# Kernel tuning notes

Measured on AMD Instinct MI355X. Metric: run time of the kernel, lower is better.

The kernel has to match this reference:

```python
import jax, jax.numpy as jnp
import numpy as np

B, T, C, H = 4, 2048, 1024, 16
HS = C // H  # head_size = 64


def setup_inputs() -> dict:
    key = jax.random.key(0)
    ks = jax.random.split(key, 6)
    s = C ** -0.5  # Linear default init scale (approx, kaiming-uniform-ish)
    x = jax.random.normal(ks[0], (B, T, C), dtype=jnp.float32)
    Wq = jax.random.normal(ks[1], (H, C, HS), dtype=jnp.float32) * s
    Wk = jax.random.normal(ks[2], (H, C, HS), dtype=jnp.float32) * s
    Wv = jax.random.normal(ks[3], (H, C, HS), dtype=jnp.float32) * s
    Wproj = jax.random.normal(ks[4], (C, C), dtype=jnp.float32) * s
    bproj = jax.random.normal(ks[5], (C,), dtype=jnp.float32) * s
    return {"x": x, "Wq": Wq, "Wk": Wk, "Wv": Wv, "Wproj": Wproj, "bproj": bproj}


def reference(x, Wq, Wk, Wv, Wproj, bproj):
    # Batched multi-head attention equivalent to looping over per-head modules.
    # q,k,v: (B, H, T, HS)
    q = jnp.einsum('btc,hcd->bhtd', x, Wq)
    k = jnp.einsum('btc,hcd->bhtd', x, Wk)
    v = jnp.einsum('btc,hcd->bhtd', x, Wv)
    scale = HS ** -0.5
    scores = jnp.einsum('bhqd,bhkd->bhqk', q, k) * scale  # (B,H,T,T)
    causal = jnp.tril(jnp.ones((T, T), dtype=bool))
    scores = jnp.where(causal, scores, -jnp.inf)
    wei = jax.nn.softmax(scores, axis=-1)
    out_heads = jnp.einsum('bhqk,bhkd->bhqd', wei, v)  # (B,H,T,HS)
    # concat heads along last dim -> (B,T,H*HS) = (B,T,C)
    combo = out_heads.transpose(0, 2, 1, 3).reshape(B, T, C)
    out = jnp.einsum('btc,cd->btd', combo, Wproj.T.T @ jnp.eye(C, dtype=combo.dtype)) if False else combo @ Wproj.T + bproj
    # dropout p=0.0 (eval) -> identity
    return out
```

## Files before the change

kernel.cpp:

```cpp
#include <hip/hip_runtime.h>
#include <stdint.h>

#define B_  4
#define T_  2048
#define C_  1024
#define H_  16
#define HS_ 64
#define M_  (B_*T_)
#define K_  C_

typedef unsigned short u16;
typedef float v4f __attribute__((ext_vector_type(4)));
typedef short v8s __attribute__((ext_vector_type(8)));
typedef u16   v4u __attribute__((ext_vector_type(4)));
typedef unsigned int u32;
typedef u32 v2u32 __attribute__((ext_vector_type(2)));

__device__ __forceinline__ u16 f2bf(float f){
  unsigned u = __float_as_uint(f);
  u += 0x7fffu + ((u >> 16) & 1u);
  return (u16)(u >> 16);
}

__device__ __forceinline__ u32 cvt_pk_bf16(float a, float b){
  u32 r;
  asm("v_cvt_pk_bf16_f32 %0, %1, %2" : "=v"(r) : "v"(a), "v"(b));
  return r;
}

__device__ __forceinline__ void async16(const void* g, void* l){
  __builtin_amdgcn_global_load_lds(
      (const __attribute__((address_space(1))) unsigned int*)g,
      (__attribute__((address_space(3))) unsigned int*)l,
      16, 0, 0);
}

__global__ void conv_f32_bf16(const float* __restrict__ src, u16* __restrict__ dst){
  int i = (blockIdx.x * 256 + threadIdx.x) * 4;
  v4f v = *(const v4f*)(src + i);
  v4u o;
  #pragma unroll
  for (int j = 0; j < 4; j++) o[j] = f2bf(v[j]);
  *(v4u*)(dst + i) = o;
}

__global__ void transpose_w(const float* __restrict__ Wq, const float* __restrict__ Wk,
                            const float* __restrict__ Wv, u16* __restrict__ wallT){
  int idx = blockIdx.x * 256 + threadIdx.x;
  int n = idx >> 10, c = idx & 1023;
  int tensor = n >> 10;
  int h = (n >> 6) & 15;
  int d = n & 63;
  const float* W = (tensor == 0) ? Wq : ((tensor == 1) ? Wk : Wv);
  wallT[idx] = f2bf(W[((size_t)(h * C_ + c)) * HS_ + d]);
}

#define QSCALE 0.1803368801111204f

template<int MODE>
__global__ __launch_bounds__(256)
void gemm_bt(const u16* __restrict__ A, const u16* __restrict__ Bt,
             const float* __restrict__ bias,
             u16* __restrict__ o0, u16* __restrict__ o1, u16* __restrict__ o2,
             float* __restrict__ o0f)
{
  __shared__ __align__(16) u16 sA[2][128 * 32];
  __shared__ __align__(16) u16 sB[2][128 * 32];
  const int tid  = threadIdx.x;
  const int lane = tid & 63;
  const int wave = tid >> 6;
  const int l15  = lane & 15, quad = lane >> 4;
  const int wm   = wave >> 1, wn = wave & 1;
  const int m0   = blockIdx.y * 128;
  const int n0   = blockIdx.x * 128;

  v4f acc[4][4] = {};

  const int s0 = tid, s1 = tid + 256;
  const int ar0 = ((s0 >> 6) << 4) + (s0 & 15);
  const int ac0 = ((s0 >> 4) & 3) << 4;
  const int ar1 = ((s1 >> 6) << 4) + (s1 & 15);
  const int ac1 = ((s1 >> 4) & 3) << 4;

  const char* Ab = (const char*)A;
  const char* Bb = (const char*)Bt;

  async16(Ab + ((size_t)(m0 + ar0) * K_) * 2 + ac0, (char*)sA[0] + s0 * 16);
  async16(Ab + ((size_t)(m0 + ar1) * K_) * 2 + ac1, (char*)sA[0] + s1 * 16);
  async16(Bb + ((size_t)(n0 + ar0) * K_) * 2 + ac0, (char*)sB[0] + s0 * 16);
  async16(Bb + ((size_t)(n0 + ar1) * K_) * 2 + ac1, (char*)sB[0] + s1 * 16);
  __syncthreads();

  int cur = 0;
  for (int kk = 0; kk < K_; kk += 32){
    const int nxt = cur ^ 1;
    if (kk + 32 < K_){
      const int k2b = (kk + 32) * 2;
      async16(Ab + ((size_t)(m0 + ar0) * K_) * 2 + k2b + ac0, (char*)sA[nxt] + s0 * 16);
      async16(Ab + ((size_t)(m0 + ar1) * K_) * 2 + k2b + ac1, (char*)sA[nxt] + s1 * 16);
      async16(Bb + ((size_t)(n0 + ar0) * K_) * 2 + k2b + ac0, (char*)sB[nxt] + s0 * 16);
      async16(Bb + ((size_t)(n0 + ar1) * K_) * 2 + k2b + ac1, (char*)sB[nxt] + s1 * 16);
    }

    v8s af[4], bfr[4];
    const u16* pa = sA[cur] + (size_t)(wm * 4) * 512 + lane * 8;
    const u16* pb = sB[cur] + (size_t)(wn * 4) * 512 + lane * 8;
    #pragma unroll
    for (int mi = 0; mi < 4; mi++) af[mi]  = *(const v8s*)(pa + mi * 512);
    #pragma unroll
    for (int ni = 0; ni < 4; ni++) bfr[ni] = *(const v8s*)(pb + ni * 512);

    #pragma unroll
    for (int mi = 0; mi < 4; mi++)
      #pragma unroll
      for (int ni = 0; ni < 4; ni++)
        acc[mi][ni] = __builtin_amdgcn_mfma_f32_16x16x32_bf16(af[mi], bfr[ni], acc[mi][ni], 0, 0, 0);

    __syncthreads();
    cur = nxt;
  }

  if constexpr (MODE == 0){
    #pragma unroll
    for (int ni = 0; ni < 4; ni++){
      const int ng = n0 + wn * 64 + ni * 16 + l15;
      const int tensor = ng >> 10;
      const int hh = (ng >> 6) & 15;
      const int d  = ng & 63;
      #pragma unroll
      for (int mi = 0; mi < 4; mi++){
        const int mbase = m0 + wm * 64 + mi * 16 + quad * 4;
        const int bb = mbase >> 11;
        const int tt = mbase & 2047;
        if (tensor == 2){
          v4u pk;
          #pragma unroll
          for (int r = 0; r < 4; r++) pk[r] = f2bf(acc[mi][ni][r]);
          *(v4u*)(o2 + ((size_t)((bb * H_ + hh) * HS_ + d)) * T_ + tt) = pk;
        } else if (tensor == 0){
          #pragma unroll
          for (int r = 0; r < 4; r++)
            o0[((size_t)((bb * H_ + hh)) * T_ + tt + r) * HS_ + d] = f2bf(acc[mi][ni][r] * QSCALE);
        } else {
          #pragma unroll
          for (int r = 0; r < 4; r++)
            o1[((size_t)((bb * H_ + hh)) * T_ + tt + r) * HS_ + d] = f2bf(acc[mi][ni][r]);
        }
      }
    }
  } else {
    #pragma unroll
    for (int ni = 0; ni < 4; ni++){
      const int ng = n0 + wn * 64 + ni * 16 + l15;
      const float bv = bias[ng];
      #pragma unroll
      for (int mi = 0; mi < 4; mi++){
        const int mbase = m0 + wm * 64 + mi * 16 + quad * 4;
        #pragma unroll
        for (int r = 0; r < 4; r++)
          o0f[(size_t)(mbase + r) * C_ + ng] = acc[mi][ni][r] + bv;
      }
    }
  }
}

__global__ __launch_bounds__(512, 4)
void attn(const u16* __restrict__ Q, const u16* __restrict__ Kb_, const u16* __restrict__ Vt,
          u16* __restrict__ O)
{
  __shared__ __align__(16) u16 sK[64 * 64];
  __shared__ __align__(16) u16 sV[64 * 64];
  __shared__ __align__(16) u16 Plds[8][16][88];
  const int tid  = threadIdx.x;
  const int lane = tid & 63;
  const int wave = tid >> 6;
  const int l15  = lane & 15, quad = lane >> 4;
  const int pp   = blockIdx.y & 7;
  const int bh   = blockIdx.x * 8 + (blockIdx.y >> 3);

  const u16* Qb = Q   + (size_t)bh * T_ * HS_;
  const u16* Kb = Kb_ + (size_t)bh * T_ * HS_;
  const u16* Vb = Vt  + (size_t)bh * HS_ * T_;
  const int b = bh >> 4, h = bh & 15;

  const int g  = tid;
  const int tg = g >> 3;
  const int sw = ((g & 7) ^ (tg & 7)) << 4;
  const char* Kby = (const char*)Kb;
  const char* Vby = (const char*)Vb;
  const int koff = tg * 128 + sw;
  const int voff = tg * (T_ * 2) + sw;
  char* sKp = (char*)sK + g * 16;
  char* sVp = (char*)sV + g * 16;

  const int fsw0 = (quad ^ (l15 & 7)) * 8;
  const int fsw1 = ((quad + 4) ^ (l15 & 7)) * 8;

  #pragma unroll 1
  for (int ph = 0; ph < 2; ph++){
    const int qt = ph ? (15 - pp) : pp;
    const int q0 = qt * 128 + wave * 16;

    const v8s qf0 = *(const v8s*)(Qb + (size_t)(q0 + l15) * HS_ + quad * 8);
    const v8s qf1 = *(const v8s*)(Qb + (size_t)(q0 + l15) * HS_ + 32 + quad * 8);

    v4f Oa[4] = {};
    float lsum = 0.f;

    const int ktmax = 2 * qt + 1;
    for (int kt = 0; kt <= ktmax; kt++){
      const int k0 = kt * 64;
      async16(Kby + (size_t)k0 * 128 + koff, sKp);
      async16(Vby + (size_t)k0 * 2   + voff, sVp);
      __syncthreads();

      if (k0 <= q0 + 15){
        v4f sacc[4] = {};
        __builtin_amdgcn_s_setprio(1);
        #pragma unroll
        for (int nt = 0; nt < 4; nt++){
          const u16* kr = sK + (nt * 16 + l15) * 64;
          v8s kf0 = *(const v8s*)(kr + fsw0);
          v8s kf1 = *(const v8s*)(kr + fsw1);
          sacc[nt] = __builtin_amdgcn_mfma_f32_16x16x32_bf16(kf0, qf0, sacc[nt], 0, 0, 0);
          sacc[nt] = __builtin_amdgcn_mfma_f32_16x16x32_bf16(kf1, qf1, sacc[nt], 0, 0, 0);
        }
        __builtin_amdgcn_s_setprio(0);
        const bool diag = (k0 + 63 > q0);
        const int qrow_rel = (q0 - k0) + l15;

        #pragma unroll
        for (int nt = 0; nt < 4; nt++){
          float p0 = exp2f(sacc[nt][0]);
          float p1 = exp2f(sacc[nt][1]);
          float p2 = exp2f(sacc[nt][2]);
          float p3 = exp2f(sacc[nt][3]);
          if (diag){
            const int kbase = nt * 16 + quad * 4;
            if (kbase + 0 > qrow_rel) p0 = 0.f;
            if (kbase + 1 > qrow_rel) p1 = 0.f;
            if (kbase + 2 > qrow_rel) p2 = 0.f;
            if (kbase + 3 > qrow_rel) p3 = 0.f;
          }
          lsum += (p0 + p1) + (p2 + p3);
          v2u32 w;
          w[0] = cvt_pk_bf16(p0, p1);
          w[1] = cvt_pk_bf16(p2, p3);
          *(v2u32*)&Plds[wave][l15][nt * 16 + quad * 4] = w;
        }

        asm volatile("" ::: "memory");
        const v8s pf0 = *(const v8s*)&Plds[wave][l15][quad * 8];
        const v8s pf1 = *(const v8s*)&Plds[wave][l15][32 + quad * 8];
        __builtin_amdgcn_s_setprio(1);
        #pragma unroll
        for (int nt = 0; nt < 4; nt++){
          const u16* vr = sV + (nt * 16 + l15) * 64;
          v8s vf0 = *(const v8s*)(vr + fsw0);
          v8s vf1 = *(const v8s*)(vr + fsw1);
          Oa[nt] = __builtin_amdgcn_mfma_f32_16x16x32_bf16(pf0, vf0, Oa[nt], 0, 0, 0);
          Oa[nt] = __builtin_amdgcn_mfma_f32_16x16x32_bf16(pf1, vf1, Oa[nt], 0, 0, 0);
        }
        __builtin_amdgcn_s_setprio(0);
      }
      __syncthreads();
    }

    float rs = lsum;
    rs += __shfl_xor(rs, 16);
    rs += __shfl_xor(rs, 32);
    #pragma unroll
    for (int reg = 0; reg < 4; reg++){
      const float rsq = __shfl(rs, quad * 4 + reg);
      const float inv = (rsq > 0.f) ? (1.f / rsq) : 0.f;
      const int t = q0 + quad * 4 + reg;
      #pragma unroll
      for (int nt = 0; nt < 4; nt++)
        O[((size_t)(b * T_ + t)) * C_ + h * HS_ + nt * 16 + l15] = f2bf(Oa[nt][reg] * inv);
    }
  }
}

extern "C" void kernel_launch(void* const* d_in, const int* in_sizes, int n_in,
                              void* d_out, int out_size, void* d_ws, size_t ws_size,
                              hipStream_t stream)
{
  const float* x     = (const float*)d_in[0];
  const float* Wq    = (const float*)d_in[1];
  const float* Wk    = (const float*)d_in[2];
  const float* Wv    = (const float*)d_in[3];
  const float* Wproj = (const float*)d_in[4];
  const float* bproj = (const float*)d_in[5];
  float* out = (float*)d_out;

  u16* xhat   = (u16*)d_ws;
  u16* att    = xhat;
  u16* q_ws   = xhat  + (size_t)M_ * C_;
  u16* k_ws   = q_ws  + (size_t)M_ * C_;
  u16* vt_ws  = k_ws  + (size_t)M_ * C_;
  u16* wallT  = vt_ws + (size_t)M_ * C_;
  u16* wprojT = wallT + (size_t)3 * C_ * K_;

  conv_f32_bf16<<<dim3((M_ * C_) / 1024), dim3(256), 0, stream>>>(x, xhat);
  transpose_w<<<dim3((3 * C_ * K_) / 256), dim3(256), 0, stream>>>(Wq, Wk, Wv, wallT);
  conv_f32_bf16<<<dim3((C_ * C_) / 1024), dim3(256), 0, stream>>>(Wproj, wprojT);
  gemm_bt<0><<<dim3(24, 64), dim3(256), 0, stream>>>(xhat, wallT, nullptr,
                                                     q_ws, k_ws, vt_ws, nullptr);
  attn<<<dim3(8, 64), dim3(512), 0, stream>>>(q_ws, k_ws, vt_ws, att);
  gemm_bt<1><<<dim3(8, 64), dim3(256), 0, stream>>>(att, wprojT, bproj,
                                                    nullptr, nullptr, nullptr, out);
}
```

Baseline: 308.3 us.

## Store GEMM operands in pre-blocked 16x8 tile layout for contiguous async loads

Changes the bf16 conversion of x and Wproj, the QKV weight transpose, and the attention output write so that operands are stored in a blocked layout: groups of 16 rows by 8 k-elements are contiguous. The GEMM's async global-to-LDS loads then read contiguous 16-byte chunks with a simple per-k-step offset, where before each load was strided by a full row. The aim is better memory coalescing and simpler address arithmetic in the GEMMs. In exchange, the attention output stores and the weight transpose now write scattered 2-byte elements, which may reduce write efficiency there.

```diff
diff --git a/kernel.cpp b/kernel.cpp
--- a/kernel.cpp
+++ b/kernel.cpp
@@ -35,13 +35,18 @@
       16, 0, 0);
 }
 
-__global__ void conv_f32_bf16(const float* __restrict__ src, u16* __restrict__ dst){
-  int i = (blockIdx.x * 256 + threadIdx.x) * 4;
-  v4f v = *(const v4f*)(src + i);
-  v4u o;
-  #pragma unroll
-  for (int j = 0; j < 4; j++) o[j] = f2bf(v[j]);
-  *(v4u*)(dst + i) = o;
+
+__global__ void conv_blocked(const float* __restrict__ src, u16* __restrict__ dst){
+  int gid = blockIdx.x * 256 + threadIdx.x;
+  int r  = gid >> 7;
+  int kg = gid & 127;
+  const float* s = src + ((size_t)r << 10) + (kg << 3);
+  v4f a = *(const v4f*)s;
+  v4f b = *(const v4f*)(s + 4);
+  union { v8s v; u16 e[8]; } o;
+  o.e[0]=f2bf(a[0]); o.e[1]=f2bf(a[1]); o.e[2]=f2bf(a[2]); o.e[3]=f2bf(a[3]);
+  o.e[4]=f2bf(b[0]); o.e[5]=f2bf(b[1]); o.e[6]=f2bf(b[2]); o.e[7]=f2bf(b[3]);
+  *(v8s*)(dst + (((size_t)(r >> 4) * 128 + kg) * 128 + ((r & 15) << 3))) = o.v;
 }
 
 __global__ void transpose_w(const float* __restrict__ Wq, const float* __restrict__ Wk,
@@ -52,7 +57,8 @@
   int h = (n >> 6) & 15;
   int d = n & 63;
   const float* W = (tensor == 0) ? Wq : ((tensor == 1) ? Wk : Wv);
-  wallT[idx] = f2bf(W[((size_t)(h * C_ + c)) * HS_ + d]);
+  wallT[((size_t)(n >> 4) * 128 + (c >> 3)) * 128 + ((n & 15) << 3) + (c & 7)]
+      = f2bf(W[((size_t)(h * C_ + c)) * HS_ + d]);
 }
 
 #define QSCALE 0.1803368801111204f
@@ -73,33 +79,35 @@
   const int wm   = wave >> 1, wn = wave & 1;
   const int m0   = blockIdx.y * 128;
   const int n0   = blockIdx.x * 128;
+  const int mg0  = blockIdx.y * 8;
+  const int ng0  = blockIdx.x * 8;
 
   v4f acc[4][4] = {};
 
   const int s0 = tid, s1 = tid + 256;
-  const int ar0 = ((s0 >> 6) << 4) + (s0 & 15);
-  const int ac0 = ((s0 >> 4) & 3) << 4;
-  const int ar1 = ((s1 >> 6) << 4) + (s1 & 15);
-  const int ac1 = ((s1 >> 4) & 3) << 4;
-
-  const char* Ab = (const char*)A;
-  const char* Bb = (const char*)Bt;
-
-  async16(Ab + ((size_t)(m0 + ar0) * K_) * 2 + ac0, (char*)sA[0] + s0 * 16);
-  async16(Ab + ((size_t)(m0 + ar1) * K_) * 2 + ac1, (char*)sA[0] + s1 * 16);
-  async16(Bb + ((size_t)(n0 + ar0) * K_) * 2 + ac0, (char*)sB[0] + s0 * 16);
-  async16(Bb + ((size_t)(n0 + ar1) * K_) * 2 + ac1, (char*)sB[0] + s1 * 16);
+  const int t0 = s0 >> 6, r0 = s0 & 15, g0 = (s0 >> 4) & 3;
+  const int t1 = s1 >> 6, r1 = s1 & 15, g1 = (s1 >> 4) & 3;
+
+  const char* aS0 = (const char*)A  + ((size_t)(mg0 + t0) * 16384 + g0 * 128 + r0 * 8) * 2;
+  const char* aS1 = (const char*)A  + ((size_t)(mg0 + t1) * 16384 + g1 * 128 + r1 * 8) * 2;
+  const char* bS0 = (const char*)Bt + ((size_t)(ng0 + t0) * 16384 + g0 * 128 + r0 * 8) * 2;
+  const char* bS1 = (const char*)Bt + ((size_t)(ng0 + t1) * 16384 + g1 * 128 + r1 * 8) * 2;
+
+  async16(aS0, (char*)sA[0] + s0 * 16);
+  async16(aS1, (char*)sA[0] + s1 * 16);
+  async16(bS0, (char*)sB[0] + s0 * 16);
+  async16(bS1, (char*)sB[0] + s1 * 16);
   __syncthreads();
 
   int cur = 0;
   for (int kk = 0; kk < K_; kk += 32){
     const int nxt = cur ^ 1;
     if (kk + 32 < K_){
-      const int k2b = (kk + 32) * 2;
-      async16(Ab + ((size_t)(m0 + ar0) * K_) * 2 + k2b + ac0, (char*)sA[nxt] + s0 * 16);
-      async16(Ab + ((size_t)(m0 + ar1) * K_) * 2 + k2b + ac1, (char*)sA[nxt] + s1 * 16);
-      async16(Bb + ((size_t)(n0 + ar0) * K_) * 2 + k2b + ac0, (char*)sB[nxt] + s0 * 16);
-      async16(Bb + ((size_t)(n0 + ar1) * K_) * 2 + k2b + ac1, (char*)sB[nxt] + s1 * 16);
+      const size_t off = (size_t)(kk + 32) * 32;
+      async16(aS0 + off, (char*)sA[nxt] + s0 * 16);
+      async16(aS1 + off, (char*)sA[nxt] + s1 * 16);
+      async16(bS0 + off, (char*)sB[nxt] + s0 * 16);
+      async16(bS1 + off, (char*)sB[nxt] + s1 * 16);
     }
 
     v8s af[4], bfr[4];
@@ -269,14 +277,17 @@
     float rs = lsum;
     rs += __shfl_xor(rs, 16);
     rs += __shfl_xor(rs, 32);
+    const int mg = b * 128 + qt * 8 + wave;
     #pragma unroll
     for (int reg = 0; reg < 4; reg++){
       const float rsq = __shfl(rs, quad * 4 + reg);
       const float inv = (rsq > 0.f) ? (1.f / rsq) : 0.f;
-      const int t = q0 + quad * 4 + reg;
+      const int mrow = quad * 4 + reg;
       #pragma unroll
-      for (int nt = 0; nt < 4; nt++)
-        O[((size_t)(b * T_ + t)) * C_ + h * HS_ + nt * 16 + l15] = f2bf(Oa[nt][reg] * inv);
+      for (int nt = 0; nt < 4; nt++){
+        const int cg = h * 8 + nt * 2 + (l15 >> 3);
+        O[((size_t)mg * 128 + cg) * 128 + mrow * 8 + (l15 & 7)] = f2bf(Oa[nt][reg] * inv);
+      }
     }
   }
 }
@@ -301,9 +312,9 @@
   u16* wallT  = vt_ws + (size_t)M_ * C_;
   u16* wprojT = wallT + (size_t)3 * C_ * K_;
 
-  conv_f32_bf16<<<dim3((M_ * C_) / 1024), dim3(256), 0, stream>>>(x, xhat);
+  conv_blocked<<<dim3((M_ * C_) / 8 / 256), dim3(256), 0, stream>>>(x, xhat);
   transpose_w<<<dim3((3 * C_ * K_) / 256), dim3(256), 0, stream>>>(Wq, Wk, Wv, wallT);
-  conv_f32_bf16<<<dim3((C_ * C_) / 1024), dim3(256), 0, stream>>>(Wproj, wprojT);
+  conv_blocked<<<dim3((C_ * C_) / 8 / 256), dim3(256), 0, stream>>>(Wproj, wprojT);
   gemm_bt<0><<<dim3(24, 64), dim3(256), 0, stream>>>(xhat, wallT, nullptr,
                                                      q_ws, k_ws, vt_ws, nullptr);
   attn<<<dim3(8, 64), dim3(512), 0, stream>>>(q_ws, k_ws, vt_ws, att);
```

Measured after the change: 270.0 us. 1.14x faster.
